# Performance work log

Hardware: AMD Instinct MI355X
Metric: run time of the kernel (lower is better)

The kernel has to match this reference:

```python
import jax, jax.numpy as jnp
import numpy as np

B, C, L = 16, 384, 4096      # batch, in_channels, sequence length
K = 4096                     # kernel_size (global 'same'-size kernel)
KH = 32                      # kernel_hidden_channels
NL = 3                       # kernel_no_layers
OMEGA = 976.0                # omega_0
HID = 384                    # net hidden_channels (pointwise out)


def setup_inputs() -> dict:
    key = jax.random.key(0)
    ks = jax.random.split(key, 10)
    s = 1.0 / np.sqrt(KH)
    return {
        "x": jax.random.normal(ks[0], (B, C, L), jnp.float32),
        # Gaussian mask parameters (learnable, init mean=0 sigma=1)
        "mask_mean": jnp.zeros((1,), jnp.float32),
        "mask_sigma": jnp.ones((1,), jnp.float32),
        # MAGNet (MFN with anisotropic Gabor filters): NL+1 filters
        "gabor_freq_w": jax.random.normal(ks[1], (NL + 1, KH, 1), jnp.float32),
        "gabor_freq_b": jax.random.uniform(ks[2], (NL + 1, KH), jnp.float32, -np.pi, np.pi),
        "gabor_gamma": jax.random.gamma(ks[3], 2.0, (NL + 1, KH, 1)).astype(jnp.float32),
        "gabor_mu": jax.random.uniform(ks[4], (NL + 1, KH, 1), jnp.float32, -1.0, 1.0),
        # NL hidden linear layers of the MFN
        "lin_w": jax.random.normal(ks[5], (NL, KH, KH), jnp.float32) * s,
        "lin_b": jnp.zeros((NL, KH), jnp.float32),
        # output linear layer (re-weighted by 1/sqrt(C*K) in forward)
        "out_w": jax.random.normal(ks[6], (C, KH), jnp.float32) * s,
        "out_b": jnp.zeros((C,), jnp.float32),
        # pointwise (1x1) conv weight, bias=False per net_cfg
        "pw_w": jax.random.normal(ks[7], (HID, C), jnp.float32) * (1.0 / np.sqrt(C)),
    }


def reference(x, mask_mean, mask_sigma, gabor_freq_w, gabor_freq_b,
              gabor_gamma, gabor_mu, lin_w, lin_b, out_w, out_b, pw_w):
    # relative positions in [-1, 1], shape [K, 1] (data_dim = 1)
    pos = jnp.linspace(-1.0, 1.0, K, dtype=x.dtype).reshape(K, 1)

    def gabor(i):
        # anisotropic Gabor filter: gaussian envelope * sinusoid
        diff = pos[:, None, :] - gabor_mu[i][None]                    # [K, KH, 1]
        env = jnp.exp(-0.5 * jnp.sum((gabor_gamma[i][None] * diff) ** 2, -1))  # [K, KH]
        sinus = jnp.sin(OMEGA * (pos @ gabor_freq_w[i].T) + gabor_freq_b[i])   # [K, KH]
        return env * sinus

    # MFN forward over kernel positions
    h = gabor(0)
    for i in range(NL):  # fixed small layer count
        h = (h @ lin_w[i].T + lin_b[i]) * gabor(i + 1)
    # re_weight_output_layer: scale output so kernel variance ~ 1/(C*K)
    scale = 1.0 / np.sqrt(C * K)
    conv_kernel = ((h @ out_w.T + out_b) * scale).T[None]             # [1, C, K]

    # learnable gaussian mask over positions -> masked kernel
    mask = jnp.exp(-0.5 * ((pos[:, 0] - mask_mean[0]) / mask_sigma[0]) ** 2)  # [K]
    masked_kernel = conv_kernel * mask[None, None, :]

    # causal FFT long convolution (K > fft_threshold -> fftconv path)
    n = L + K  # linear (non-circular) convolution length
    y = jnp.fft.irfft(jnp.fft.rfft(x, n=n) * jnp.fft.rfft(masked_kernel, n=n), n=n)[..., :L]

    # pointwise 1x1 conv, bias=False
    out = jnp.einsum('bcl,oc->bol', y, pw_w)
    return out
```

## Files before the change

kernel.cpp:

```cpp
#include <hip/hip_runtime.h>
#include <math.h>

#define B_    16
#define C_    384
#define L_    4096
#define K_    4096
#define KH_   32
#define NL_   3
#define HID_  384
#define NFFT  8192
#define NH    4096
#define OMEGA_ 976.0f

__global__ __launch_bounds__(256) void gen_tw(float2* __restrict__ tw) {
  int j = blockIdx.x * 256 + threadIdx.x;
  if (j < NH) {
    double a = -2.0 * 3.14159265358979323846 * (double)j / (double)NFFT;
    double s, c;
    sincos(a, &s, &c);
    tw[j] = make_float2((float)c, (float)s);
  }
}

__global__ __launch_bounds__(256) void gen_mk(
    const float* __restrict__ mask_mean, const float* __restrict__ mask_sigma,
    const float* __restrict__ gfw, const float* __restrict__ gfb,
    const float* __restrict__ gg,  const float* __restrict__ gmu,
    const float* __restrict__ lin_w, const float* __restrict__ lin_b,
    const float* __restrict__ out_w, const float* __restrict__ out_b,
    float* __restrict__ mk) {
  __shared__ float s_h[256][KH_ + 1];
  __shared__ float s_ms[256];
  const int t = threadIdx.x;
  const int k = blockIdx.x * 256 + t;
  const float xp = -1.0f + 2.0f * (float)k / (float)(K_ - 1);

  float h[KH_];
  #pragma unroll
  for (int j = 0; j < KH_; ++j) {
    float d   = gg[j] * (xp - gmu[j]);
    float env = expf(-0.5f * d * d);
    float su  = sinf(OMEGA_ * (xp * gfw[j]) + gfb[j]);
    h[j] = env * su;
  }
  for (int i = 0; i < NL_; ++i) {
    const float* lw = lin_w + i * KH_ * KH_;
    const int go = (i + 1) * KH_;
    float nh[KH_];
    #pragma unroll
    for (int h2 = 0; h2 < KH_; ++h2) {
      float acc = lin_b[i * KH_ + h2];
      #pragma unroll
      for (int j = 0; j < KH_; ++j) acc = fmaf(h[j], lw[h2 * KH_ + j], acc);
      float d   = gg[go + h2] * (xp - gmu[go + h2]);
      float env = expf(-0.5f * d * d);
      float su  = sinf(OMEGA_ * (xp * gfw[go + h2]) + gfb[go + h2]);
      nh[h2] = acc * (env * su);
    }
    #pragma unroll
    for (int j = 0; j < KH_; ++j) h[j] = nh[j];
  }
  float mw = (xp - mask_mean[0]) / mask_sigma[0];
  float ms = expf(-0.5f * mw * mw) * rsqrtf((float)(C_ * K_));
  s_ms[t] = ms;
  #pragma unroll
  for (int j = 0; j < KH_; ++j) s_h[t][j] = h[j] * ms;
  __syncthreads();

  for (int c = 0; c < C_; ++c) {
    float acc = out_b[c] * s_ms[t];
    #pragma unroll
    for (int j = 0; j < KH_; ++j) acc = fmaf(s_h[t][j], out_w[c * KH_ + j], acc);
    mk[(size_t)c * K_ + k] = acc;
  }
}

__device__ __forceinline__ void fft_dif(float2* z, const float2* __restrict__ tw, int tid) {
  for (int m = NH; m >= 1; m >>= 1) {
    const int stride = NH / m;
    for (int idx = tid; idx < NH; idx += 256) {
      int j = idx & (m - 1);
      int p = ((idx - j) << 1) + j;
      float2 a = z[p], b = z[p + m];
      z[p] = make_float2(a.x + b.x, a.y + b.y);
      float trr = a.x - b.x, tii = a.y - b.y;
      float2 w = tw[j * stride];
      z[p + m] = make_float2(trr * w.x - tii * w.y, trr * w.y + tii * w.x);
    }
    __syncthreads();
  }
}

__device__ __forceinline__ void fft_dit_inv(float2* z, const float2* __restrict__ tw, int tid) {
  for (int m = 1; m <= NH; m <<= 1) {
    const int stride = NH / m;
    for (int idx = tid; idx < NH; idx += 256) {
      int j = idx & (m - 1);
      int p = ((idx - j) << 1) + j;
      float2 w = tw[j * stride];
      float wr = w.x, wi = -w.y;
      float2 b = z[p + m];
      float trr = b.x * wr - b.y * wi;
      float tii = b.x * wi + b.y * wr;
      float2 a = z[p];
      z[p]     = make_float2(a.x + trr, a.y + tii);
      z[p + m] = make_float2(a.x - trr, a.y - tii);
    }
    __syncthreads();
  }
}

__global__ __launch_bounds__(256) void fft_h(const float* __restrict__ mk,
                                             const float2* __restrict__ tw,
                                             float2* __restrict__ Hspec) {
  extern __shared__ float2 z[];
  const int c = blockIdx.x;
  const int tid = threadIdx.x;
  const float* row = mk + (size_t)c * K_;
  for (int i = tid; i < K_; i += 256) {
    z[i]      = make_float2(row[i], 0.0f);
    z[i + K_] = make_float2(0.0f, 0.0f);
  }
  __syncthreads();
  fft_dif(z, tw, tid);
  const float inv = 1.0f / (float)NFFT;
  float2* outp = Hspec + (size_t)c * NFFT;
  for (int i = tid; i < NFFT; i += 256) {
    float2 v = z[i];
    outp[i] = make_float2(v.x * inv, v.y * inv);
  }
}

__global__ __launch_bounds__(256) void fft_conv(const float* __restrict__ x,
                                                const float2* __restrict__ Hspec,
                                                const float2* __restrict__ tw,
                                                float* __restrict__ y) {
  extern __shared__ float2 z[];
  const int c  = blockIdx.x % C_;
  const int pr = blockIdx.x / C_;
  const int b1 = 2 * pr, b2 = b1 + 1;
  const int tid = threadIdx.x;
  const float4* x1 = reinterpret_cast<const float4*>(x + ((size_t)b1 * C_ + c) * L_);
  const float4* x2 = reinterpret_cast<const float4*>(x + ((size_t)b2 * C_ + c) * L_);
  for (int i = tid; i < L_ / 4; i += 256) {
    float4 a = x1[i], b = x2[i];
    int p = i * 4;
    z[p]          = make_float2(a.x, b.x);
    z[p + 1]      = make_float2(a.y, b.y);
    z[p + 2]      = make_float2(a.z, b.z);
    z[p + 3]      = make_float2(a.w, b.w);
    z[p + L_]     = make_float2(0.f, 0.f);
    z[p + L_ + 1] = make_float2(0.f, 0.f);
    z[p + L_ + 2] = make_float2(0.f, 0.f);
    z[p + L_ + 3] = make_float2(0.f, 0.f);
  }
  __syncthreads();
  fft_dif(z, tw, tid);
  const float2* H = Hspec + (size_t)c * NFFT;
  for (int i = tid; i < NFFT; i += 256) {
    float2 h = H[i];
    float2 v = z[i];
    z[i] = make_float2(v.x * h.x - v.y * h.y, v.x * h.y + v.y * h.x);
  }
  __syncthreads();
  fft_dit_inv(z, tw, tid);
  float4* y1 = reinterpret_cast<float4*>(y + ((size_t)b1 * C_ + c) * L_);
  float4* y2 = reinterpret_cast<float4*>(y + ((size_t)b2 * C_ + c) * L_);
  for (int i = tid; i < L_ / 4; i += 256) {
    int p = i * 4;
    float2 v0 = z[p], v1 = z[p + 1], v2 = z[p + 2], v3 = z[p + 3];
    y1[i] = make_float4(v0.x, v1.x, v2.x, v3.x);
    y2[i] = make_float4(v0.y, v1.y, v2.y, v3.y);
  }
}

#define MT 64
#define NT 64
#define KT 16
__global__ __launch_bounds__(256) void pw_gemm(const float* __restrict__ y,
                                               const float* __restrict__ pw,
                                               float* __restrict__ out) {
  const int b  = blockIdx.z;
  const int m0 = blockIdx.y * MT;
  const int n0 = blockIdx.x * NT;
  __shared__ float As[KT][MT + 4];
  __shared__ float Bs[KT][NT + 4];
  const int tid = threadIdx.x;
  const int tx = tid & 15, ty = tid >> 4;
  float acc[4][4] = {{0.f}};
  const float* yb = y + (size_t)b * C_ * L_;

  for (int k0 = 0; k0 < C_; k0 += KT) {
    {
      int r = tid >> 2, c4 = (tid & 3) << 2;
      float4 av = *reinterpret_cast<const float4*>(pw + (size_t)(m0 + r) * C_ + k0 + c4);
      As[c4 + 0][r] = av.x; As[c4 + 1][r] = av.y;
      As[c4 + 2][r] = av.z; As[c4 + 3][r] = av.w;
    }
    {
      int r = ty, cc = tx << 2;
      float4 bv = *reinterpret_cast<const float4*>(yb + (size_t)(k0 + r) * L_ + n0 + cc);
      *reinterpret_cast<float4*>(&Bs[r][cc]) = bv;
    }
    __syncthreads();
    #pragma unroll
    for (int kk = 0; kk < KT; ++kk) {
      float4 a  = *reinterpret_cast<const float4*>(&As[kk][ty << 2]);
      float4 bv = *reinterpret_cast<const float4*>(&Bs[kk][tx << 2]);
      float av[4] = {a.x, a.y, a.z, a.w};
      float bb[4] = {bv.x, bv.y, bv.z, bv.w};
      #pragma unroll
      for (int i = 0; i < 4; ++i)
        #pragma unroll
        for (int j = 0; j < 4; ++j)
          acc[i][j] = fmaf(av[i], bb[j], acc[i][j]);
    }
    __syncthreads();
  }
  float* ob = out + ((size_t)b * HID_ + m0) * L_ + n0;
  #pragma unroll
  for (int i = 0; i < 4; ++i) {
    float4 v = make_float4(acc[i][0], acc[i][1], acc[i][2], acc[i][3]);
    *reinterpret_cast<float4*>(ob + (size_t)(ty * 4 + i) * L_ + tx * 4) = v;
  }
}

extern "C" void kernel_launch(void* const* d_in, const int* in_sizes, int n_in,
                              void* d_out, int out_size, void* d_ws, size_t ws_size,
                              hipStream_t stream) {
  (void)in_sizes; (void)n_in; (void)out_size; (void)ws_size;
  const float* x          = (const float*)d_in[0];
  const float* mask_mean  = (const float*)d_in[1];
  const float* mask_sigma = (const float*)d_in[2];
  const float* gfw        = (const float*)d_in[3];
  const float* gfb        = (const float*)d_in[4];
  const float* gg         = (const float*)d_in[5];
  const float* gmu        = (const float*)d_in[6];
  const float* lin_w      = (const float*)d_in[7];
  const float* lin_b      = (const float*)d_in[8];
  const float* out_w      = (const float*)d_in[9];
  const float* out_b      = (const float*)d_in[10];
  const float* pw_w       = (const float*)d_in[11];
  float* out = (float*)d_out;

  char* ws = (char*)d_ws;
  float2* tw = (float2*)ws;
  float*  mk = (float*)(ws + 32768);
  float2* Hs = (float2*)(ws + 32768 + 6291456);
  float*  y  = (float*)(ws + 32768 + 6291456 + 25165824);

  gen_tw<<<NH / 256, 256, 0, stream>>>(tw);
  gen_mk<<<K_ / 256, 256, 0, stream>>>(mask_mean, mask_sigma, gfw, gfb, gg, gmu,
                                       lin_w, lin_b, out_w, out_b, mk);
  fft_h<<<C_, 256, NFFT * sizeof(float2), stream>>>(mk, tw, Hs);
  fft_conv<<<(B_ / 2) * C_, 256, NFFT * sizeof(float2), stream>>>(x, Hs, tw, y);
  pw_gemm<<<dim3(L_ / 64, HID_ / 64, B_), 256, 0, stream>>>(y, pw_w, out);
}
```

Before: 1.017 ms.

## Replace radix-2 FFT with radix-8/16 split-array FFT, retile GEMM, parallelize kernel gen

The shared-memory FFT changes from 13 radix-2 stages, each ending in a barrier, to three radix-8 stages plus a final radix-16 pass held in registers. That pass is fused with the spectral multiply and the first inverse pass, and the data moves to separate real and imaginary arrays with an XOR swizzle to avoid bank conflicts. The pointwise GEMM tile grows from 64x64 to 128x128 so each thread computes an 8x8 block, and gen_mk is spread over a second grid dimension of channel groups. This cuts synchronizations and LDS traffic and raises FMA reuse in the GEMM, at the cost of more registers, which may lower occupancy, and recomputing the MFN in each channel-group block.

```diff
diff --git a/kernel.cpp b/kernel.cpp
--- a/kernel.cpp
+++ b/kernel.cpp
@@ -9,17 +9,133 @@
 #define NL_   3
 #define HID_  384
 #define NFFT  8192
-#define NH    4096
 #define OMEGA_ 976.0f
+
+#define SWZ(a) ((a) ^ ((((a) >> 7) & 1) << 4))
 
 __global__ __launch_bounds__(256) void gen_tw(float2* __restrict__ tw) {
   int j = blockIdx.x * 256 + threadIdx.x;
-  if (j < NH) {
+  if (j < NFFT) {
     double a = -2.0 * 3.14159265358979323846 * (double)j / (double)NFFT;
     double s, c;
     sincos(a, &s, &c);
     tw[j] = make_float2((float)c, (float)s);
   }
+}
+
+__device__ __forceinline__ float2 cadd(float2 a, float2 b) { return make_float2(a.x + b.x, a.y + b.y); }
+__device__ __forceinline__ float2 csub(float2 a, float2 b) { return make_float2(a.x - b.x, a.y - b.y); }
+__device__ __forceinline__ float2 cmul(float2 a, float2 b) { return make_float2(a.x * b.x - a.y * b.y, a.x * b.y + a.y * b.x); }
+__device__ __forceinline__ float2 cmulc(float2 a, float2 b) {
+  return make_float2(a.x * b.x + a.y * b.y, a.y * b.x - a.x * b.y);
+}
+
+__device__ __forceinline__ void dft8_fwd(float2* a) {
+  const float c = 0.70710678118654752f;
+  float2 t0 = cadd(a[0], a[4]), t1 = csub(a[0], a[4]);
+  float2 t2 = cadd(a[2], a[6]), t3 = csub(a[2], a[6]);
+  float2 t4 = cadd(a[1], a[5]), t5 = csub(a[1], a[5]);
+  float2 t6 = cadd(a[3], a[7]), t7 = csub(a[3], a[7]);
+  float2 E0 = cadd(t0, t2), E2 = csub(t0, t2);
+  float2 E1 = make_float2(t1.x + t3.y, t1.y - t3.x);
+  float2 E3 = make_float2(t1.x - t3.y, t1.y + t3.x);
+  float2 O0 = cadd(t4, t6), O2 = csub(t4, t6);
+  float2 O1 = make_float2(t5.x + t7.y, t5.y - t7.x);
+  float2 O3 = make_float2(t5.x - t7.y, t5.y + t7.x);
+  float2 O1w = make_float2(c * (O1.x + O1.y), c * (O1.y - O1.x));
+  float2 O2w = make_float2(O2.y, -O2.x);
+  float2 O3w = make_float2(c * (O3.y - O3.x), -c * (O3.x + O3.y));
+  a[0] = cadd(E0, O0);  a[4] = csub(E0, O0);
+  a[1] = cadd(E1, O1w); a[5] = csub(E1, O1w);
+  a[2] = cadd(E2, O2w); a[6] = csub(E2, O2w);
+  a[3] = cadd(E3, O3w); a[7] = csub(E3, O3w);
+}
+
+__device__ __forceinline__ void dft8_inv(float2* a) {
+  const float c = 0.70710678118654752f;
+  float2 t0 = cadd(a[0], a[4]), t1 = csub(a[0], a[4]);
+  float2 t2 = cadd(a[2], a[6]), t3 = csub(a[2], a[6]);
+  float2 t4 = cadd(a[1], a[5]), t5 = csub(a[1], a[5]);
+  float2 t6 = cadd(a[3], a[7]), t7 = csub(a[3], a[7]);
+  float2 E0 = cadd(t0, t2), E2 = csub(t0, t2);
+  float2 E1 = make_float2(t1.x - t3.y, t1.y + t3.x);
+  float2 E3 = make_float2(t1.x + t3.y, t1.y - t3.x);
+  float2 O0 = cadd(t4, t6), O2 = csub(t4, t6);
+  float2 O1 = make_float2(t5.x - t7.y, t5.y + t7.x);
+  float2 O3 = make_float2(t5.x + t7.y, t5.y - t7.x);
+  float2 O1w = make_float2(c * (O1.x - O1.y), c * (O1.x + O1.y));
+  float2 O2w = make_float2(-O2.y, O2.x);
+  float2 O3w = make_float2(-c * (O3.x + O3.y), c * (O3.x - O3.y));
+  a[0] = cadd(E0, O0);  a[4] = csub(E0, O0);
+  a[1] = cadd(E1, O1w); a[5] = csub(E1, O1w);
+  a[2] = cadd(E2, O2w); a[6] = csub(E2, O2w);
+  a[3] = cadd(E3, O3w); a[7] = csub(E3, O3w);
+}
+
+template <bool INV>
+__device__ __forceinline__ void stage8(float* zr, float* zi, const float2* __restrict__ tw,
+                                       int tid, int d, int ld, int stride) {
+  #pragma unroll
+  for (int rep = 0; rep < 4; ++rep) {
+    int idx = tid + rep * 256;
+    int j = idx & (d - 1);
+    int p = ((idx >> ld) << (ld + 3)) + j;
+    float2 v[8];
+    #pragma unroll
+    for (int t = 0; t < 8; ++t) { int q = SWZ(p + t * d); v[t] = make_float2(zr[q], zi[q]); }
+    if (INV) {
+      #pragma unroll
+      for (int k = 1; k < 8; ++k) v[k] = cmulc(v[k], tw[j * k * stride]);
+      dft8_inv(v);
+    } else {
+      dft8_fwd(v);
+      #pragma unroll
+      for (int k = 1; k < 8; ++k) v[k] = cmul(v[k], tw[j * k * stride]);
+    }
+    #pragma unroll
+    for (int t = 0; t < 8; ++t) { int q = SWZ(p + t * d); zr[q] = v[t].x; zi[q] = v[t].y; }
+  }
+  __syncthreads();
+}
+
+__device__ __forceinline__ void reg16_fwd(float2* v, const float2* __restrict__ tw) {
+  float2 t[8];
+  #pragma unroll
+  for (int k = 0; k < 8; ++k) t[k] = v[2 * k];
+  dft8_fwd(t);
+  #pragma unroll
+  for (int k = 0; k < 8; ++k) v[2 * k] = t[k];
+  #pragma unroll
+  for (int k = 0; k < 8; ++k) t[k] = v[2 * k + 1];
+  dft8_fwd(t);
+  #pragma unroll
+  for (int k = 1; k < 8; ++k) t[k] = cmul(t[k], tw[k * 512]);
+  #pragma unroll
+  for (int k = 0; k < 8; ++k) v[2 * k + 1] = t[k];
+  #pragma unroll
+  for (int q = 0; q < 8; ++q) {
+    float2 a = v[2 * q], b = v[2 * q + 1];
+    v[2 * q] = cadd(a, b); v[2 * q + 1] = csub(a, b);
+  }
+}
+
+__device__ __forceinline__ void reg16_inv(float2* v, const float2* __restrict__ tw) {
+  #pragma unroll
+  for (int q = 0; q < 8; ++q) {
+    float2 a = v[2 * q], b = v[2 * q + 1];
+    v[2 * q] = cadd(a, b); v[2 * q + 1] = csub(a, b);
+  }
+  float2 t[8];
+  #pragma unroll
+  for (int k = 0; k < 8; ++k) t[k] = v[2 * k];
+  dft8_inv(t);
+  #pragma unroll
+  for (int k = 0; k < 8; ++k) v[2 * k] = t[k];
+  #pragma unroll
+  for (int k = 0; k < 8; ++k) t[k] = cmulc(v[2 * k + 1], tw[k * 512]);
+  dft8_inv(t);
+  #pragma unroll
+  for (int k = 0; k < 8; ++k) v[2 * k + 1] = t[k];
 }
 
 __global__ __launch_bounds__(256) void gen_mk(
@@ -29,10 +145,9 @@
     const float* __restrict__ lin_w, const float* __restrict__ lin_b,
     const float* __restrict__ out_w, const float* __restrict__ out_b,
     float* __restrict__ mk) {
-  __shared__ float s_h[256][KH_ + 1];
-  __shared__ float s_ms[256];
   const int t = threadIdx.x;
   const int k = blockIdx.x * 256 + t;
+  const int c0 = blockIdx.y * 16;
   const float xp = -1.0f + 2.0f * (float)k / (float)(K_ - 1);
 
   float h[KH_];
@@ -62,72 +177,59 @@
   }
   float mw = (xp - mask_mean[0]) / mask_sigma[0];
   float ms = expf(-0.5f * mw * mw) * rsqrtf((float)(C_ * K_));
-  s_ms[t] = ms;
-  #pragma unroll
-  for (int j = 0; j < KH_; ++j) s_h[t][j] = h[j] * ms;
-  __syncthreads();
-
-  for (int c = 0; c < C_; ++c) {
-    float acc = out_b[c] * s_ms[t];
-    #pragma unroll
-    for (int j = 0; j < KH_; ++j) acc = fmaf(s_h[t][j], out_w[c * KH_ + j], acc);
+  #pragma unroll
+  for (int j = 0; j < KH_; ++j) h[j] *= ms;
+
+  for (int cc = 0; cc < 16; ++cc) {
+    int c = c0 + cc;
+    float acc = out_b[c] * ms;
+    #pragma unroll
+    for (int j = 0; j < KH_; ++j) acc = fmaf(h[j], out_w[c * KH_ + j], acc);
     mk[(size_t)c * K_ + k] = acc;
-  }
-}
-
-__device__ __forceinline__ void fft_dif(float2* z, const float2* __restrict__ tw, int tid) {
-  for (int m = NH; m >= 1; m >>= 1) {
-    const int stride = NH / m;
-    for (int idx = tid; idx < NH; idx += 256) {
-      int j = idx & (m - 1);
-      int p = ((idx - j) << 1) + j;
-      float2 a = z[p], b = z[p + m];
-      z[p] = make_float2(a.x + b.x, a.y + b.y);
-      float trr = a.x - b.x, tii = a.y - b.y;
-      float2 w = tw[j * stride];
-      z[p + m] = make_float2(trr * w.x - tii * w.y, trr * w.y + tii * w.x);
-    }
-    __syncthreads();
-  }
-}
-
-__device__ __forceinline__ void fft_dit_inv(float2* z, const float2* __restrict__ tw, int tid) {
-  for (int m = 1; m <= NH; m <<= 1) {
-    const int stride = NH / m;
-    for (int idx = tid; idx < NH; idx += 256) {
-      int j = idx & (m - 1);
-      int p = ((idx - j) << 1) + j;
-      float2 w = tw[j * stride];
-      float wr = w.x, wi = -w.y;
-      float2 b = z[p + m];
-      float trr = b.x * wr - b.y * wi;
-      float tii = b.x * wi + b.y * wr;
-      float2 a = z[p];
-      z[p]     = make_float2(a.x + trr, a.y + tii);
-      z[p + m] = make_float2(a.x - trr, a.y - tii);
-    }
-    __syncthreads();
   }
 }
 
 __global__ __launch_bounds__(256) void fft_h(const float* __restrict__ mk,
                                              const float2* __restrict__ tw,
                                              float2* __restrict__ Hspec) {
-  extern __shared__ float2 z[];
+  extern __shared__ float smem[];
+  float* zr = smem;
+  float* zi = smem + NFFT;
   const int c = blockIdx.x;
   const int tid = threadIdx.x;
-  const float* row = mk + (size_t)c * K_;
-  for (int i = tid; i < K_; i += 256) {
-    z[i]      = make_float2(row[i], 0.0f);
-    z[i + K_] = make_float2(0.0f, 0.0f);
+  const float4* row4 = reinterpret_cast<const float4*>(mk + (size_t)c * K_);
+  const float4 z4 = make_float4(0.f, 0.f, 0.f, 0.f);
+  for (int i = tid; i < K_ / 4; i += 256) {
+    int p = i * 4;
+    *reinterpret_cast<float4*>(&zr[SWZ(p)]) = row4[i];
+    *reinterpret_cast<float4*>(&zi[SWZ(p)]) = z4;
+    *reinterpret_cast<float4*>(&zr[SWZ(p + K_)]) = z4;
+    *reinterpret_cast<float4*>(&zi[SWZ(p + K_)]) = z4;
   }
   __syncthreads();
-  fft_dif(z, tw, tid);
+  stage8<false>(zr, zi, tw, tid, 1024, 10, 1);
+  stage8<false>(zr, zi, tw, tid, 128, 7, 8);
+  stage8<false>(zr, zi, tw, tid, 16, 4, 64);
+
   const float inv = 1.0f / (float)NFFT;
   float2* outp = Hspec + (size_t)c * NFFT;
-  for (int i = tid; i < NFFT; i += 256) {
-    float2 v = z[i];
-    outp[i] = make_float2(v.x * inv, v.y * inv);
+  #pragma unroll
+  for (int rep = 0; rep < 2; ++rep) {
+    int cb = tid + rep * 256;
+    int base = cb * 16, pb = SWZ(base);
+    float2 v[16];
+    #pragma unroll
+    for (int q4 = 0; q4 < 4; ++q4) {
+      float4 re = *reinterpret_cast<const float4*>(&zr[pb + q4 * 4]);
+      float4 im = *reinterpret_cast<const float4*>(&zi[pb + q4 * 4]);
+      v[q4 * 4 + 0] = make_float2(re.x, im.x);
+      v[q4 * 4 + 1] = make_float2(re.y, im.y);
+      v[q4 * 4 + 2] = make_float2(re.z, im.z);
+      v[q4 * 4 + 3] = make_float2(re.w, im.w);
+    }
+    reg16_fwd(v, tw);
+    #pragma unroll
+    for (int q = 0; q < 16; ++q) outp[base + q] = make_float2(v[q].x * inv, v[q].y * inv);
   }
 }
 
@@ -135,94 +237,136 @@
                                                 const float2* __restrict__ Hspec,
                                                 const float2* __restrict__ tw,
                                                 float* __restrict__ y) {
-  extern __shared__ float2 z[];
+  extern __shared__ float smem[];
+  float* zr = smem;
+  float* zi = smem + NFFT;
   const int c  = blockIdx.x % C_;
   const int pr = blockIdx.x / C_;
   const int b1 = 2 * pr, b2 = b1 + 1;
   const int tid = threadIdx.x;
   const float4* x1 = reinterpret_cast<const float4*>(x + ((size_t)b1 * C_ + c) * L_);
   const float4* x2 = reinterpret_cast<const float4*>(x + ((size_t)b2 * C_ + c) * L_);
+  const float4 z4 = make_float4(0.f, 0.f, 0.f, 0.f);
   for (int i = tid; i < L_ / 4; i += 256) {
-    float4 a = x1[i], b = x2[i];
     int p = i * 4;
-    z[p]          = make_float2(a.x, b.x);
-    z[p + 1]      = make_float2(a.y, b.y);
-    z[p + 2]      = make_float2(a.z, b.z);
-    z[p + 3]      = make_float2(a.w, b.w);
-    z[p + L_]     = make_float2(0.f, 0.f);
-    z[p + L_ + 1] = make_float2(0.f, 0.f);
-    z[p + L_ + 2] = make_float2(0.f, 0.f);
-    z[p + L_ + 3] = make_float2(0.f, 0.f);
+    *reinterpret_cast<float4*>(&zr[SWZ(p)]) = x1[i];
+    *reinterpret_cast<float4*>(&zi[SWZ(p)]) = x2[i];
+    *reinterpret_cast<float4*>(&zr[SWZ(p + L_)]) = z4;
+    *reinterpret_cast<float4*>(&zi[SWZ(p + L_)]) = z4;
   }
   __syncthreads();
-  fft_dif(z, tw, tid);
-  const float2* H = Hspec + (size_t)c * NFFT;
-  for (int i = tid; i < NFFT; i += 256) {
-    float2 h = H[i];
-    float2 v = z[i];
-    z[i] = make_float2(v.x * h.x - v.y * h.y, v.x * h.y + v.y * h.x);
+  stage8<false>(zr, zi, tw, tid, 1024, 10, 1);
+  stage8<false>(zr, zi, tw, tid, 128, 7, 8);
+  stage8<false>(zr, zi, tw, tid, 16, 4, 64);
+
+  const float2* Hc = Hspec + (size_t)c * NFFT;
+  #pragma unroll
+  for (int rep = 0; rep < 2; ++rep) {
+    int cb = tid + rep * 256;
+    int base = cb * 16, pb = SWZ(base);
+    float2 v[16];
+    #pragma unroll
+    for (int q4 = 0; q4 < 4; ++q4) {
+      float4 re = *reinterpret_cast<const float4*>(&zr[pb + q4 * 4]);
+      float4 im = *reinterpret_cast<const float4*>(&zi[pb + q4 * 4]);
+      v[q4 * 4 + 0] = make_float2(re.x, im.x);
+      v[q4 * 4 + 1] = make_float2(re.y, im.y);
+      v[q4 * 4 + 2] = make_float2(re.z, im.z);
+      v[q4 * 4 + 3] = make_float2(re.w, im.w);
+    }
+    reg16_fwd(v, tw);
+    #pragma unroll
+    for (int q = 0; q < 16; ++q) v[q] = cmul(v[q], Hc[base + q]);
+    reg16_inv(v, tw);
+    #pragma unroll
+    for (int q4 = 0; q4 < 4; ++q4) {
+      float4 re = make_float4(v[q4 * 4 + 0].x, v[q4 * 4 + 1].x, v[q4 * 4 + 2].x, v[q4 * 4 + 3].x);
+      float4 im = make_float4(v[q4 * 4 + 0].y, v[q4 * 4 + 1].y, v[q4 * 4 + 2].y, v[q4 * 4 + 3].y);
+      *reinterpret_cast<float4*>(&zr[pb + q4 * 4]) = re;
+      *reinterpret_cast<float4*>(&zi[pb + q4 * 4]) = im;
+    }
   }
   __syncthreads();
-  fft_dit_inv(z, tw, tid);
+  stage8<true>(zr, zi, tw, tid, 16, 4, 64);
+  stage8<true>(zr, zi, tw, tid, 128, 7, 8);
+  stage8<true>(zr, zi, tw, tid, 1024, 10, 1);
+
   float4* y1 = reinterpret_cast<float4*>(y + ((size_t)b1 * C_ + c) * L_);
   float4* y2 = reinterpret_cast<float4*>(y + ((size_t)b2 * C_ + c) * L_);
   for (int i = tid; i < L_ / 4; i += 256) {
     int p = i * 4;
-    float2 v0 = z[p], v1 = z[p + 1], v2 = z[p + 2], v3 = z[p + 3];
-    y1[i] = make_float4(v0.x, v1.x, v2.x, v3.x);
-    y2[i] = make_float4(v0.y, v1.y, v2.y, v3.y);
-  }
-}
-
-#define MT 64
-#define NT 64
+    y1[i] = *reinterpret_cast<const float4*>(&zr[SWZ(p)]);
+    y2[i] = *reinterpret_cast<const float4*>(&zi[SWZ(p)]);
+  }
+}
+
+#define MT 128
+#define NT 128
 #define KT 16
+#define LDT 132
 __global__ __launch_bounds__(256) void pw_gemm(const float* __restrict__ y,
                                                const float* __restrict__ pw,
                                                float* __restrict__ out) {
   const int b  = blockIdx.z;
   const int m0 = blockIdx.y * MT;
   const int n0 = blockIdx.x * NT;
-  __shared__ float As[KT][MT + 4];
-  __shared__ float Bs[KT][NT + 4];
+  __shared__ float As[KT][LDT];
+  __shared__ float Bs[KT][LDT];
   const int tid = threadIdx.x;
   const int tx = tid & 15, ty = tid >> 4;
-  float acc[4][4] = {{0.f}};
+  float acc[2][2][4][4] = {{{{0.f}}}};
   const float* yb = y + (size_t)b * C_ * L_;
 
   for (int k0 = 0; k0 < C_; k0 += KT) {
-    {
-      int r = tid >> 2, c4 = (tid & 3) << 2;
-      float4 av = *reinterpret_cast<const float4*>(pw + (size_t)(m0 + r) * C_ + k0 + c4);
-      As[c4 + 0][r] = av.x; As[c4 + 1][r] = av.y;
-      As[c4 + 2][r] = av.z; As[c4 + 3][r] = av.w;
-    }
-    {
-      int r = ty, cc = tx << 2;
+    #pragma unroll
+    for (int rep = 0; rep < 2; ++rep) {
+      int idx = tid + rep * 256;
+      int row = idx >> 2, c4 = (idx & 3) << 2;
+      float4 av = *reinterpret_cast<const float4*>(pw + (size_t)(m0 + row) * C_ + k0 + c4);
+      As[c4 + 0][row] = av.x; As[c4 + 1][row] = av.y;
+      As[c4 + 2][row] = av.z; As[c4 + 3][row] = av.w;
+    }
+    #pragma unroll
+    for (int rep = 0; rep < 2; ++rep) {
+      int idx = tid + rep * 256;
+      int r = idx >> 5, cc = (idx & 31) << 2;
       float4 bv = *reinterpret_cast<const float4*>(yb + (size_t)(k0 + r) * L_ + n0 + cc);
       *reinterpret_cast<float4*>(&Bs[r][cc]) = bv;
     }
     __syncthreads();
     #pragma unroll
     for (int kk = 0; kk < KT; ++kk) {
-      float4 a  = *reinterpret_cast<const float4*>(&As[kk][ty << 2]);
-      float4 bv = *reinterpret_cast<const float4*>(&Bs[kk][tx << 2]);
-      float av[4] = {a.x, a.y, a.z, a.w};
-      float bb[4] = {bv.x, bv.y, bv.z, bv.w};
+      float4 a0 = *reinterpret_cast<const float4*>(&As[kk][ty * 4]);
+      float4 a1 = *reinterpret_cast<const float4*>(&As[kk][ty * 4 + 64]);
+      float4 b0 = *reinterpret_cast<const float4*>(&Bs[kk][tx * 4]);
+      float4 b1 = *reinterpret_cast<const float4*>(&Bs[kk][tx * 4 + 64]);
+      float av[2][4] = {{a0.x, a0.y, a0.z, a0.w}, {a1.x, a1.y, a1.z, a1.w}};
+      float bv[2][4] = {{b0.x, b0.y, b0.z, b0.w}, {b1.x, b1.y, b1.z, b1.w}};
       #pragma unroll
-      for (int i = 0; i < 4; ++i)
+      for (int ri = 0; ri < 2; ++ri)
         #pragma unroll
-        for (int j = 0; j < 4; ++j)
-          acc[i][j] = fmaf(av[i], bb[j], acc[i][j]);
+        for (int rj = 0; rj < 2; ++rj)
+          #pragma unroll
+          for (int i = 0; i < 4; ++i)
+            #pragma unroll
+            for (int j = 0; j < 4; ++j)
+              acc[ri][rj][i][j] = fmaf(av[ri][i], bv[rj][j], acc[ri][rj][i][j]);
     }
     __syncthreads();
   }
-  float* ob = out + ((size_t)b * HID_ + m0) * L_ + n0;
-  #pragma unroll
-  for (int i = 0; i < 4; ++i) {
-    float4 v = make_float4(acc[i][0], acc[i][1], acc[i][2], acc[i][3]);
-    *reinterpret_cast<float4*>(ob + (size_t)(ty * 4 + i) * L_ + tx * 4) = v;
-  }
+  #pragma unroll
+  for (int ri = 0; ri < 2; ++ri)
+    #pragma unroll
+    for (int i = 0; i < 4; ++i) {
+      int grow = m0 + ty * 4 + i + ri * 64;
+      float* orow = out + ((size_t)b * HID_ + grow) * L_ + n0;
+      #pragma unroll
+      for (int rj = 0; rj < 2; ++rj) {
+        float4 v = make_float4(acc[ri][rj][i][0], acc[ri][rj][i][1],
+                               acc[ri][rj][i][2], acc[ri][rj][i][3]);
+        *reinterpret_cast<float4*>(orow + tx * 4 + rj * 64) = v;
+      }
+    }
 }
 
 extern "C" void kernel_launch(void* const* d_in, const int* in_sizes, int n_in,
@@ -245,14 +389,14 @@
 
   char* ws = (char*)d_ws;
   float2* tw = (float2*)ws;
-  float*  mk = (float*)(ws + 32768);
-  float2* Hs = (float2*)(ws + 32768 + 6291456);
-  float*  y  = (float*)(ws + 32768 + 6291456 + 25165824);
-
-  gen_tw<<<NH / 256, 256, 0, stream>>>(tw);
-  gen_mk<<<K_ / 256, 256, 0, stream>>>(mask_mean, mask_sigma, gfw, gfb, gg, gmu,
-                                       lin_w, lin_b, out_w, out_b, mk);
-  fft_h<<<C_, 256, NFFT * sizeof(float2), stream>>>(mk, tw, Hs);
-  fft_conv<<<(B_ / 2) * C_, 256, NFFT * sizeof(float2), stream>>>(x, Hs, tw, y);
-  pw_gemm<<<dim3(L_ / 64, HID_ / 64, B_), 256, 0, stream>>>(y, pw_w, out);
-}
+  float*  mk = (float*)(ws + 65536);
+  float2* Hs = (float2*)(ws + 65536 + 6291456);
+  float*  y  = (float*)(ws + 65536 + 6291456 + 25165824);
+
+  gen_tw<<<NFFT / 256, 256, 0, stream>>>(tw);
+  gen_mk<<<dim3(K_ / 256, 24), 256, 0, stream>>>(mask_mean, mask_sigma, gfw, gfb, gg, gmu,
+                                                 lin_w, lin_b, out_w, out_b, mk);
+  fft_h<<<C_, 256, 2 * NFFT * sizeof(float), stream>>>(mk, tw, Hs);
+  fft_conv<<<(B_ / 2) * C_, 256, 2 * NFFT * sizeof(float), stream>>>(x, Hs, tw, y);
+  pw_gemm<<<dim3(L_ / NT, HID_ / MT, B_), 256, 0, stream>>>(y, pw_w, out);
+}
```

Result: faster. 844.7 us (-16.9%).
